# Kernel optimization log

Hardware: AMD Instinct MI355X
Metric: run time of the kernel (lower is better)

The kernel has to match this reference:

```python
import jax, jax.numpy as jnp
import numpy as np

E = 8
HID = 2048
INTER = 1408
TOT = 8192


def setup_inputs() -> dict:
    key = jax.random.key(0)
    k1, k2, k3, k4, k5 = jax.random.split(key, 5)
    # uneven token counts per expert that sum exactly to TOT (grouped-GEMM ragged sizes)
    deltas = np.array([512, -256, 128, -384, 256, -512, 384, -128], dtype=np.int32)
    tokens_per_expert = jnp.asarray(TOT // E + deltas, dtype=jnp.int32)  # sums to TOT
    permuted_x = jax.random.normal(k1, (TOT, HID), dtype=jnp.float32)
    permuted_probs = jax.random.uniform(k2, (TOT,), dtype=jnp.float32)
    s_in = 1.0 / np.sqrt(HID)
    s_mid = 1.0 / np.sqrt(INTER)
    w_gate = jax.random.normal(k3, (E, HID, INTER), dtype=jnp.float32) * s_in
    w_up = jax.random.normal(k4, (E, HID, INTER), dtype=jnp.float32) * s_in
    w_down = jax.random.normal(k5, (E, INTER, HID), dtype=jnp.float32) * s_mid
    return {
        "permuted_x": permuted_x,
        "permuted_probs": permuted_probs,
        "w_gate": w_gate,
        "w_up": w_up,
        "w_down": w_down,
        "tokens_per_expert": tokens_per_expert,
    }


def reference(permuted_x, permuted_probs, w_gate, w_up, w_down, tokens_per_expert):
    # Grouped GEMM: tokens sorted by expert; lax.ragged_dot contracts each
    # contiguous group of rows against its expert's weight without padding.
    gate = jax.lax.ragged_dot(permuted_x, w_gate, tokens_per_expert)  # [T, INTER]
    up = jax.lax.ragged_dot(permuted_x, w_up, tokens_per_expert)      # [T, INTER]
    h = jax.nn.silu(gate) * up                                         # fused SiLU-mul
    values = jax.lax.ragged_dot(h, w_down, tokens_per_expert)          # [T, HID]
    return permuted_probs[:, None].astype(values.dtype) * values
```

## Files before the change

### kernel.cpp

```cpp
#include <hip/hip_runtime.h>

typedef unsigned short u16;
typedef unsigned int u32;
typedef u16 us8 __attribute__((ext_vector_type(8)));
typedef __bf16 bf16x8 __attribute__((ext_vector_type(8)));
typedef float f32x4 __attribute__((ext_vector_type(4)));

constexpr int kE = 8;
constexpr int kHID = 2048;
constexpr int kINTER = 1408;
constexpr int kTOT = 8192;

static __device__ __forceinline__ u16 f2bf(float f) {
  u32 u = __float_as_uint(f);
  u32 r = (u + 0x7fffu + ((u >> 16) & 1u)) >> 16;
  return (u16)r;
}

static __device__ __forceinline__ void gll16(const u16* g, u16* l) {
  __builtin_amdgcn_global_load_lds(
      (const __attribute__((address_space(1))) u32*)g,
      (__attribute__((address_space(3))) u32*)l, 16, 0, 0);
}

__global__ void conv_bf16(const float* __restrict__ x, u16* __restrict__ o) {
  size_t i = ((size_t)blockIdx.x * 256 + threadIdx.x) * 8;
  const float4* p = (const float4*)(x + i);
  float4 f0 = p[0], f1 = p[1];
  us8 v;
  v[0] = f2bf(f0.x); v[1] = f2bf(f0.y); v[2] = f2bf(f0.z); v[3] = f2bf(f0.w);
  v[4] = f2bf(f1.x); v[5] = f2bf(f1.y); v[6] = f2bf(f1.z); v[7] = f2bf(f1.w);
  *(us8*)(o + i) = v;
}

__global__ void transp_bf16(const float* __restrict__ w, u16* __restrict__ wt,
                            int K, int N) {
  __shared__ float tile[64][65];
  int e = blockIdx.z;
  const float* we = w + (size_t)e * K * N;
  u16* wte = wt + (size_t)e * K * N;
  int n0 = blockIdx.x * 64, k0 = blockIdx.y * 64;
  int t = threadIdx.x;
  int kl = t >> 4, n4 = (t & 15) * 4;
#pragma unroll
  for (int r = 0; r < 4; r++) {
    int k = r * 16 + kl;
    float4 v = *(const float4*)(we + (size_t)(k0 + k) * N + n0 + n4);
    tile[k][n4 + 0] = v.x; tile[k][n4 + 1] = v.y;
    tile[k][n4 + 2] = v.z; tile[k][n4 + 3] = v.w;
  }
  __syncthreads();
#pragma unroll
  for (int r = 0; r < 2; r++) {
    int c = r * 256 + t;
    int n = c >> 3, kc = (c & 7) * 8;
    us8 o;
#pragma unroll
    for (int j = 0; j < 8; j++) o[j] = f2bf(tile[kc + j][n]);
    *(us8*)(wte + (size_t)(n0 + n) * K + k0 + kc) = o;
  }
}

static __device__ __forceinline__ bool expert_of_tile(
    const int* __restrict__ tpe, int ty, int& e, int& m0, int& m_end) {
  int tile_base = 0, row_base = 0;
  e = -1;
  for (int i = 0; i < kE; i++) {
    int tc = tpe[i];
    int nt = (tc + 127) >> 7;
    if (e < 0 && ty < tile_base + nt) {
      e = i;
      m0 = row_base + (ty - tile_base) * 128;
      m_end = row_base + tc;
    }
    tile_base += nt;
    row_base += tc;
  }
  return e >= 0;
}

__launch_bounds__(256, 2)
__global__ void gemm1(const u16* __restrict__ Xb, const u16* __restrict__ Wgt,
                      const u16* __restrict__ Wut, const float* __restrict__ probs,
                      const int* __restrict__ tpe, u16* __restrict__ H) {
  __shared__ __align__(16) u16 As[128 * 32];
  __shared__ __align__(16) u16 Bgs[128 * 32];
  __shared__ __align__(16) u16 Bus[128 * 32];

  int e, m0, m_end;
  if (!expert_of_tile(tpe, blockIdx.y, e, m0, m_end)) return;
  int n0 = blockIdx.x * 128;

  int t = threadIdx.x;
  int w = t >> 6, lane = t & 63;
  int quad = lane >> 4, l15 = lane & 15;
  int wm = (w >> 1) * 64, wn = (w & 1) * 64;

  int ar0 = m0 + (t >> 2);      if (ar0 > kTOT - 1) ar0 = kTOT - 1;
  int ar1 = m0 + 64 + (t >> 2); if (ar1 > kTOT - 1) ar1 = kTOT - 1;
  const u16* gA0 = Xb + (size_t)ar0 * kHID + (t & 3) * 8;
  const u16* gA1 = Xb + (size_t)ar1 * kHID + (t & 3) * 8;
  size_t wbase = ((size_t)e * kINTER + n0 + (t >> 2)) * kHID + (t & 3) * 8;
  const u16* gBg0 = Wgt + wbase;
  const u16* gBg1 = gBg0 + (size_t)64 * kHID;
  const u16* gBu0 = Wut + wbase;
  const u16* gBu1 = gBu0 + (size_t)64 * kHID;
  u16* lA0 = As + (size_t)(w * 64) * 8;
  u16* lA1 = As + (size_t)(256 + w * 64) * 8;
  u16* lBg0 = Bgs + (size_t)(w * 64) * 8;
  u16* lBg1 = Bgs + (size_t)(256 + w * 64) * 8;
  u16* lBu0 = Bus + (size_t)(w * 64) * 8;
  u16* lBu1 = Bus + (size_t)(256 + w * 64) * 8;

  int aoff[4], boff[4];
#pragma unroll
  for (int i = 0; i < 4; i++) aoff[i] = (wm + i * 16 + l15) * 32 + quad * 8;
#pragma unroll
  for (int j = 0; j < 4; j++) boff[j] = (wn + j * 16 + l15) * 32 + quad * 8;

  f32x4 accg[4][4] = {};
  f32x4 accu[4][4] = {};

  for (int kt = 0; kt < kHID / 32; kt++) {
    gll16(gA0, lA0);  gll16(gA1, lA1);
    gll16(gBg0, lBg0); gll16(gBg1, lBg1);
    gll16(gBu0, lBu0); gll16(gBu1, lBu1);
    gA0 += 32; gA1 += 32; gBg0 += 32; gBg1 += 32; gBu0 += 32; gBu1 += 32;
    __syncthreads();

    bf16x8 a[4], bg[4], bu[4];
#pragma unroll
    for (int i = 0; i < 4; i++) a[i] = *(const bf16x8*)(As + aoff[i]);
#pragma unroll
    for (int j = 0; j < 4; j++) {
      bg[j] = *(const bf16x8*)(Bgs + boff[j]);
      bu[j] = *(const bf16x8*)(Bus + boff[j]);
    }
#pragma unroll
    for (int i = 0; i < 4; i++)
#pragma unroll
      for (int j = 0; j < 4; j++) {
        accg[i][j] = __builtin_amdgcn_mfma_f32_16x16x32_bf16(a[i], bg[j], accg[i][j], 0, 0, 0);
        accu[i][j] = __builtin_amdgcn_mfma_f32_16x16x32_bf16(a[i], bu[j], accu[i][j], 0, 0, 0);
      }
    __syncthreads();
  }

#pragma unroll
  for (int i = 0; i < 4; i++) {
#pragma unroll
    for (int r = 0; r < 4; r++) {
      int row = m0 + wm + i * 16 + quad * 4 + r;
      if (row < m_end) {
        float p = probs[row];
#pragma unroll
        for (int j = 0; j < 4; j++) {
          int col = n0 + wn + j * 16 + l15;
          float g = accg[i][j][r], u = accu[i][j][r];
          float s = g / (1.0f + __expf(-g));
          H[(size_t)row * kINTER + col] = f2bf(s * u * p);
        }
      }
    }
  }
}

__launch_bounds__(256, 2)
__global__ void gemm2(const u16* __restrict__ H, const u16* __restrict__ Wdt,
                      const int* __restrict__ tpe, float* __restrict__ out) {
  __shared__ __align__(16) u16 As[128 * 32];
  __shared__ __align__(16) u16 Bs[128 * 32];

  int e, m0, m_end;
  if (!expert_of_tile(tpe, blockIdx.y, e, m0, m_end)) return;
  int n0 = blockIdx.x * 128;

  int t = threadIdx.x;
  int w = t >> 6, lane = t & 63;
  int quad = lane >> 4, l15 = lane & 15;
  int wm = (w >> 1) * 64, wn = (w & 1) * 64;

  int ar0 = m0 + (t >> 2);      if (ar0 > kTOT - 1) ar0 = kTOT - 1;
  int ar1 = m0 + 64 + (t >> 2); if (ar1 > kTOT - 1) ar1 = kTOT - 1;
  const u16* gA0 = H + (size_t)ar0 * kINTER + (t & 3) * 8;
  const u16* gA1 = H + (size_t)ar1 * kINTER + (t & 3) * 8;
  const u16* gB0 = Wdt + ((size_t)e * kHID + n0 + (t >> 2)) * kINTER + (t & 3) * 8;
  const u16* gB1 = gB0 + (size_t)64 * kINTER;
  u16* lA0 = As + (size_t)(w * 64) * 8;
  u16* lA1 = As + (size_t)(256 + w * 64) * 8;
  u16* lB0 = Bs + (size_t)(w * 64) * 8;
  u16* lB1 = Bs + (size_t)(256 + w * 64) * 8;

  int aoff[4], boff[4];
#pragma unroll
  for (int i = 0; i < 4; i++) aoff[i] = (wm + i * 16 + l15) * 32 + quad * 8;
#pragma unroll
  for (int j = 0; j < 4; j++) boff[j] = (wn + j * 16 + l15) * 32 + quad * 8;

  f32x4 acc[4][4] = {};

  for (int kt = 0; kt < kINTER / 32; kt++) {
    gll16(gA0, lA0); gll16(gA1, lA1);
    gll16(gB0, lB0); gll16(gB1, lB1);
    gA0 += 32; gA1 += 32; gB0 += 32; gB1 += 32;
    __syncthreads();

    bf16x8 a[4], b[4];
#pragma unroll
    for (int i = 0; i < 4; i++) a[i] = *(const bf16x8*)(As + aoff[i]);
#pragma unroll
    for (int j = 0; j < 4; j++) b[j] = *(const bf16x8*)(Bs + boff[j]);
#pragma unroll
    for (int i = 0; i < 4; i++)
#pragma unroll
      for (int j = 0; j < 4; j++)
        acc[i][j] = __builtin_amdgcn_mfma_f32_16x16x32_bf16(a[i], b[j], acc[i][j], 0, 0, 0);
    __syncthreads();
  }

#pragma unroll
  for (int i = 0; i < 4; i++) {
#pragma unroll
    for (int r = 0; r < 4; r++) {
      int row = m0 + wm + i * 16 + quad * 4 + r;
      if (row < m_end) {
#pragma unroll
        for (int j = 0; j < 4; j++) {
          int col = n0 + wn + j * 16 + l15;
          out[(size_t)row * kHID + col] = acc[i][j][r];
        }
      }
    }
  }
}

extern "C" void kernel_launch(void* const* d_in, const int* in_sizes, int n_in,
                              void* d_out, int out_size, void* d_ws, size_t ws_size,
                              hipStream_t stream) {
  const float* x = (const float*)d_in[0];
  const float* probs = (const float*)d_in[1];
  const float* wg = (const float*)d_in[2];
  const float* wu = (const float*)d_in[3];
  const float* wd = (const float*)d_in[4];
  const int* tpe = (const int*)d_in[5];
  float* out = (float*)d_out;

  u16* ws = (u16*)d_ws;
  u16* Xb = ws;
  u16* Wgt = Xb + (size_t)kTOT * kHID;
  u16* Wut = Wgt + (size_t)kE * kINTER * kHID;
  u16* Wdt = Wut + (size_t)kE * kINTER * kHID;
  u16* H = Wdt + (size_t)kE * kHID * kINTER;

  conv_bf16<<<(kTOT * kHID) / (256 * 8), 256, 0, stream>>>(x, Xb);
  transp_bf16<<<dim3(kINTER / 64, kHID / 64, kE), 256, 0, stream>>>(wg, Wgt, kHID, kINTER);
  transp_bf16<<<dim3(kINTER / 64, kHID / 64, kE), 256, 0, stream>>>(wu, Wut, kHID, kINTER);
  transp_bf16<<<dim3(kHID / 64, kINTER / 64, kE), 256, 0, stream>>>(wd, Wdt, kINTER, kHID);

  gemm1<<<dim3(kINTER / 128, 72), 256, 0, stream>>>(Xb, Wgt, Wut, probs, tpe, H);
  gemm2<<<dim3(kHID / 128, 72), 256, 0, stream>>>(H, Wdt, tpe, out);
}
```

Baseline: 571.0 us.

## Enlarge grouped GEMM tiles with 512-thread blocks for better operand reuse

Both grouped GEMMs now run eight waves per block. gemm1 uses a 256-row M tile against 128 gate/up columns, and gemm2 uses a 128x256 output tile. The global-to-LDS load mapping is rewritten so each wave fills 16 contiguous rows, and the tile-to-expert mapping takes a configurable tile height. The goal is to cut redundant weight and activation reloads per FLOP. The trade-offs are fewer blocks, which can hurt occupancy and load balance across CUs, and more ragged padding waste per expert with the 256-row tiles.

```diff
diff --git a/kernel.cpp b/kernel.cpp
--- a/kernel.cpp
+++ b/kernel.cpp
@@ -62,15 +62,16 @@
 }
 
 static __device__ __forceinline__ bool expert_of_tile(
-    const int* __restrict__ tpe, int ty, int& e, int& m0, int& m_end) {
+    const int* __restrict__ tpe, int ty, int tile_rows,
+    int& e, int& m0, int& m_end) {
   int tile_base = 0, row_base = 0;
   e = -1;
   for (int i = 0; i < kE; i++) {
     int tc = tpe[i];
-    int nt = (tc + 127) >> 7;
+    int nt = (tc + tile_rows - 1) / tile_rows;
     if (e < 0 && ty < tile_base + nt) {
       e = i;
-      m0 = row_base + (ty - tile_base) * 128;
+      m0 = row_base + (ty - tile_base) * tile_rows;
       m_end = row_base + tc;
     }
     tile_base += nt;
@@ -79,16 +80,16 @@
   return e >= 0;
 }
 
-__launch_bounds__(256, 2)
+__launch_bounds__(512, 2)
 __global__ void gemm1(const u16* __restrict__ Xb, const u16* __restrict__ Wgt,
                       const u16* __restrict__ Wut, const float* __restrict__ probs,
                       const int* __restrict__ tpe, u16* __restrict__ H) {
-  __shared__ __align__(16) u16 As[128 * 32];
+  __shared__ __align__(16) u16 As[256 * 32];
   __shared__ __align__(16) u16 Bgs[128 * 32];
   __shared__ __align__(16) u16 Bus[128 * 32];
 
   int e, m0, m_end;
-  if (!expert_of_tile(tpe, blockIdx.y, e, m0, m_end)) return;
+  if (!expert_of_tile(tpe, blockIdx.y, 256, e, m0, m_end)) return;
   int n0 = blockIdx.x * 128;
 
   int t = threadIdx.x;
@@ -96,21 +97,20 @@
   int quad = lane >> 4, l15 = lane & 15;
   int wm = (w >> 1) * 64, wn = (w & 1) * 64;
 
-  int ar0 = m0 + (t >> 2);      if (ar0 > kTOT - 1) ar0 = kTOT - 1;
-  int ar1 = m0 + 64 + (t >> 2); if (ar1 > kTOT - 1) ar1 = kTOT - 1;
-  const u16* gA0 = Xb + (size_t)ar0 * kHID + (t & 3) * 8;
-  const u16* gA1 = Xb + (size_t)ar1 * kHID + (t & 3) * 8;
-  size_t wbase = ((size_t)e * kINTER + n0 + (t >> 2)) * kHID + (t & 3) * 8;
-  const u16* gBg0 = Wgt + wbase;
-  const u16* gBg1 = gBg0 + (size_t)64 * kHID;
-  const u16* gBu0 = Wut + wbase;
-  const u16* gBu1 = gBu0 + (size_t)64 * kHID;
-  u16* lA0 = As + (size_t)(w * 64) * 8;
-  u16* lA1 = As + (size_t)(256 + w * 64) * 8;
-  u16* lBg0 = Bgs + (size_t)(w * 64) * 8;
-  u16* lBg1 = Bgs + (size_t)(256 + w * 64) * 8;
-  u16* lBu0 = Bus + (size_t)(w * 64) * 8;
-  u16* lBu1 = Bus + (size_t)(256 + w * 64) * 8;
+  int rl = w * 16 + (lane >> 2);
+  int kc8 = (lane & 3) * 8;
+
+  int ar0 = m0 + rl;        if (ar0 > kTOT - 1) ar0 = kTOT - 1;
+  int ar1 = m0 + 128 + rl;  if (ar1 > kTOT - 1) ar1 = kTOT - 1;
+  const u16* gA0 = Xb + (size_t)ar0 * kHID + kc8;
+  const u16* gA1 = Xb + (size_t)ar1 * kHID + kc8;
+  size_t wbase = ((size_t)e * kINTER + n0 + rl) * kHID + kc8;
+  const u16* gBg = Wgt + wbase;
+  const u16* gBu = Wut + wbase;
+  u16* lA0 = As + (size_t)(w * 16) * 32;
+  u16* lA1 = As + (size_t)(128 + w * 16) * 32;
+  u16* lBg = Bgs + (size_t)(w * 16) * 32;
+  u16* lBu = Bus + (size_t)(w * 16) * 32;
 
   int aoff[4], boff[4];
 #pragma unroll
@@ -122,10 +122,9 @@
   f32x4 accu[4][4] = {};
 
   for (int kt = 0; kt < kHID / 32; kt++) {
-    gll16(gA0, lA0);  gll16(gA1, lA1);
-    gll16(gBg0, lBg0); gll16(gBg1, lBg1);
-    gll16(gBu0, lBu0); gll16(gBu1, lBu1);
-    gA0 += 32; gA1 += 32; gBg0 += 32; gBg1 += 32; gBu0 += 32; gBu1 += 32;
+    gll16(gA0, lA0); gll16(gA1, lA1);
+    gll16(gBg, lBg); gll16(gBu, lBu);
+    gA0 += 32; gA1 += 32; gBg += 32; gBu += 32;
     __syncthreads();
 
     bf16x8 a[4], bg[4], bu[4];
@@ -165,31 +164,31 @@
   }
 }
 
-__launch_bounds__(256, 2)
+__launch_bounds__(512, 2)
 __global__ void gemm2(const u16* __restrict__ H, const u16* __restrict__ Wdt,
                       const int* __restrict__ tpe, float* __restrict__ out) {
   __shared__ __align__(16) u16 As[128 * 32];
-  __shared__ __align__(16) u16 Bs[128 * 32];
+  __shared__ __align__(16) u16 Bs[256 * 32];
 
   int e, m0, m_end;
-  if (!expert_of_tile(tpe, blockIdx.y, e, m0, m_end)) return;
-  int n0 = blockIdx.x * 128;
+  if (!expert_of_tile(tpe, blockIdx.y, 128, e, m0, m_end)) return;
+  int n0 = blockIdx.x * 256;
 
   int t = threadIdx.x;
   int w = t >> 6, lane = t & 63;
   int quad = lane >> 4, l15 = lane & 15;
-  int wm = (w >> 1) * 64, wn = (w & 1) * 64;
-
-  int ar0 = m0 + (t >> 2);      if (ar0 > kTOT - 1) ar0 = kTOT - 1;
-  int ar1 = m0 + 64 + (t >> 2); if (ar1 > kTOT - 1) ar1 = kTOT - 1;
-  const u16* gA0 = H + (size_t)ar0 * kINTER + (t & 3) * 8;
-  const u16* gA1 = H + (size_t)ar1 * kINTER + (t & 3) * 8;
-  const u16* gB0 = Wdt + ((size_t)e * kHID + n0 + (t >> 2)) * kINTER + (t & 3) * 8;
-  const u16* gB1 = gB0 + (size_t)64 * kINTER;
-  u16* lA0 = As + (size_t)(w * 64) * 8;
-  u16* lA1 = As + (size_t)(256 + w * 64) * 8;
-  u16* lB0 = Bs + (size_t)(w * 64) * 8;
-  u16* lB1 = Bs + (size_t)(256 + w * 64) * 8;
+  int wm = (w >> 2) * 64, wn = (w & 3) * 64;
+
+  int rl = w * 16 + (lane >> 2);
+  int kc8 = (lane & 3) * 8;
+
+  int ar = m0 + rl; if (ar > kTOT - 1) ar = kTOT - 1;
+  const u16* gA = H + (size_t)ar * kINTER + kc8;
+  const u16* gB0 = Wdt + ((size_t)e * kHID + n0 + rl) * kINTER + kc8;
+  const u16* gB1 = gB0 + (size_t)128 * kINTER;
+  u16* lA = As + (size_t)(w * 16) * 32;
+  u16* lB0 = Bs + (size_t)(w * 16) * 32;
+  u16* lB1 = Bs + (size_t)(128 + w * 16) * 32;
 
   int aoff[4], boff[4];
 #pragma unroll
@@ -200,9 +199,9 @@
   f32x4 acc[4][4] = {};
 
   for (int kt = 0; kt < kINTER / 32; kt++) {
-    gll16(gA0, lA0); gll16(gA1, lA1);
+    gll16(gA, lA);
     gll16(gB0, lB0); gll16(gB1, lB1);
-    gA0 += 32; gA1 += 32; gB0 += 32; gB1 += 32;
+    gA += 32; gB0 += 32; gB1 += 32;
     __syncthreads();
 
     bf16x8 a[4], b[4];
@@ -257,6 +256,6 @@
   transp_bf16<<<dim3(kINTER / 64, kHID / 64, kE), 256, 0, stream>>>(wu, Wut, kHID, kINTER);
   transp_bf16<<<dim3(kHID / 64, kINTER / 64, kE), 256, 0, stream>>>(wd, Wdt, kINTER, kHID);
 
-  gemm1<<<dim3(kINTER / 128, 72), 256, 0, stream>>>(Xb, Wgt, Wut, probs, tpe, H);
-  gemm2<<<dim3(kHID / 128, 72), 256, 0, stream>>>(H, Wdt, tpe, out);
-}
+  gemm1<<<dim3(kINTER / 128, 40), 512, 0, stream>>>(Xb, Wgt, Wut, probs, tpe, H);
+  gemm2<<<dim3(kHID / 256, 72), 512, 0, stream>>>(H, Wdt, tpe, out);
+}
```

After: 575.5 us. Within noise of the previous version (+0.8%).

## Double-buffer LDS tiles in both grouped GEMMs and raise occupancy hints

Applied to the files above, without the earlier changes.

Both GEMM kernels now keep two LDS buffers per operand. The next K-slice's global-to-LDS loads are issued right after the barrier, so they overlap the MFMA work on the current slice, and the trailing barrier is removed, leaving one sync per iteration. Launch bounds are raised to 3 blocks/CU for gemm1 and 4 for gemm2 to encourage more resident waves. The cost is double the LDS footprint and a tighter register budget, which may cause spills in gemm1 with its two accumulator sets.

```diff
diff --git a/kernel.cpp b/kernel.cpp
--- a/kernel.cpp
+++ b/kernel.cpp
@@ -79,13 +79,14 @@
   return e >= 0;
 }
 
-__launch_bounds__(256, 2)
+__launch_bounds__(256, 3)
 __global__ void gemm1(const u16* __restrict__ Xb, const u16* __restrict__ Wgt,
                       const u16* __restrict__ Wut, const float* __restrict__ probs,
                       const int* __restrict__ tpe, u16* __restrict__ H) {
-  __shared__ __align__(16) u16 As[128 * 32];
-  __shared__ __align__(16) u16 Bgs[128 * 32];
-  __shared__ __align__(16) u16 Bus[128 * 32];
+  constexpr int TE = 128 * 32;
+  __shared__ __align__(16) u16 As[2 * TE];
+  __shared__ __align__(16) u16 Bgs[2 * TE];
+  __shared__ __align__(16) u16 Bus[2 * TE];
 
   int e, m0, m_end;
   if (!expert_of_tile(tpe, blockIdx.y, e, m0, m_end)) return;
@@ -105,12 +106,12 @@
   const u16* gBg1 = gBg0 + (size_t)64 * kHID;
   const u16* gBu0 = Wut + wbase;
   const u16* gBu1 = gBu0 + (size_t)64 * kHID;
-  u16* lA0 = As + (size_t)(w * 64) * 8;
-  u16* lA1 = As + (size_t)(256 + w * 64) * 8;
-  u16* lBg0 = Bgs + (size_t)(w * 64) * 8;
-  u16* lBg1 = Bgs + (size_t)(256 + w * 64) * 8;
-  u16* lBu0 = Bus + (size_t)(w * 64) * 8;
-  u16* lBu1 = Bus + (size_t)(256 + w * 64) * 8;
+  u16* lA0 = As + w * 512;
+  u16* lA1 = As + 2048 + w * 512;
+  u16* lBg0 = Bgs + w * 512;
+  u16* lBg1 = Bgs + 2048 + w * 512;
+  u16* lBu0 = Bus + w * 512;
+  u16* lBu1 = Bus + 2048 + w * 512;
 
   int aoff[4], boff[4];
 #pragma unroll
@@ -121,20 +122,29 @@
   f32x4 accg[4][4] = {};
   f32x4 accu[4][4] = {};
 
-  for (int kt = 0; kt < kHID / 32; kt++) {
-    gll16(gA0, lA0);  gll16(gA1, lA1);
-    gll16(gBg0, lBg0); gll16(gBg1, lBg1);
-    gll16(gBu0, lBu0); gll16(gBu1, lBu1);
-    gA0 += 32; gA1 += 32; gBg0 += 32; gBg1 += 32; gBu0 += 32; gBu1 += 32;
+  gll16(gA0, lA0); gll16(gA1, lA1);
+  gll16(gBg0, lBg0); gll16(gBg1, lBg1);
+  gll16(gBu0, lBu0); gll16(gBu1, lBu1);
+  gA0 += 32; gA1 += 32; gBg0 += 32; gBg1 += 32; gBu0 += 32; gBu1 += 32;
+
+  constexpr int KT = kHID / 32;
+  for (int kt = 0; kt < KT; kt++) {
+    int cur = (kt & 1) ? TE : 0;
+    int nxt = TE - cur;
     __syncthreads();
-
+    if (kt + 1 < KT) {
+      gll16(gA0, lA0 + nxt); gll16(gA1, lA1 + nxt);
+      gll16(gBg0, lBg0 + nxt); gll16(gBg1, lBg1 + nxt);
+      gll16(gBu0, lBu0 + nxt); gll16(gBu1, lBu1 + nxt);
+      gA0 += 32; gA1 += 32; gBg0 += 32; gBg1 += 32; gBu0 += 32; gBu1 += 32;
+    }
     bf16x8 a[4], bg[4], bu[4];
 #pragma unroll
-    for (int i = 0; i < 4; i++) a[i] = *(const bf16x8*)(As + aoff[i]);
+    for (int i = 0; i < 4; i++) a[i] = *(const bf16x8*)(As + cur + aoff[i]);
 #pragma unroll
     for (int j = 0; j < 4; j++) {
-      bg[j] = *(const bf16x8*)(Bgs + boff[j]);
-      bu[j] = *(const bf16x8*)(Bus + boff[j]);
+      bg[j] = *(const bf16x8*)(Bgs + cur + boff[j]);
+      bu[j] = *(const bf16x8*)(Bus + cur + boff[j]);
     }
 #pragma unroll
     for (int i = 0; i < 4; i++)
@@ -143,7 +153,6 @@
         accg[i][j] = __builtin_amdgcn_mfma_f32_16x16x32_bf16(a[i], bg[j], accg[i][j], 0, 0, 0);
         accu[i][j] = __builtin_amdgcn_mfma_f32_16x16x32_bf16(a[i], bu[j], accu[i][j], 0, 0, 0);
       }
-    __syncthreads();
   }
 
 #pragma unroll
@@ -165,11 +174,12 @@
   }
 }
 
-__launch_bounds__(256, 2)
+__launch_bounds__(256, 4)
 __global__ void gemm2(const u16* __restrict__ H, const u16* __restrict__ Wdt,
                       const int* __restrict__ tpe, float* __restrict__ out) {
-  __shared__ __align__(16) u16 As[128 * 32];
-  __shared__ __align__(16) u16 Bs[128 * 32];
+  constexpr int TE = 128 * 32;
+  __shared__ __align__(16) u16 As[2 * TE];
+  __shared__ __align__(16) u16 Bs[2 * TE];
 
   int e, m0, m_end;
   if (!expert_of_tile(tpe, blockIdx.y, e, m0, m_end)) return;
@@ -186,10 +196,10 @@
   const u16* gA1 = H + (size_t)ar1 * kINTER + (t & 3) * 8;
   const u16* gB0 = Wdt + ((size_t)e * kHID + n0 + (t >> 2)) * kINTER + (t & 3) * 8;
   const u16* gB1 = gB0 + (size_t)64 * kINTER;
-  u16* lA0 = As + (size_t)(w * 64) * 8;
-  u16* lA1 = As + (size_t)(256 + w * 64) * 8;
-  u16* lB0 = Bs + (size_t)(w * 64) * 8;
-  u16* lB1 = Bs + (size_t)(256 + w * 64) * 8;
+  u16* lA0 = As + w * 512;
+  u16* lA1 = As + 2048 + w * 512;
+  u16* lB0 = Bs + w * 512;
+  u16* lB1 = Bs + 2048 + w * 512;
 
   int aoff[4], boff[4];
 #pragma unroll
@@ -199,23 +209,30 @@
 
   f32x4 acc[4][4] = {};
 
-  for (int kt = 0; kt < kINTER / 32; kt++) {
-    gll16(gA0, lA0); gll16(gA1, lA1);
-    gll16(gB0, lB0); gll16(gB1, lB1);
-    gA0 += 32; gA1 += 32; gB0 += 32; gB1 += 32;
+  gll16(gA0, lA0); gll16(gA1, lA1);
+  gll16(gB0, lB0); gll16(gB1, lB1);
+  gA0 += 32; gA1 += 32; gB0 += 32; gB1 += 32;
+
+  constexpr int KT = kINTER / 32;
+  for (int kt = 0; kt < KT; kt++) {
+    int cur = (kt & 1) ? TE : 0;
+    int nxt = TE - cur;
     __syncthreads();
-
+    if (kt + 1 < KT) {
+      gll16(gA0, lA0 + nxt); gll16(gA1, lA1 + nxt);
+      gll16(gB0, lB0 + nxt); gll16(gB1, lB1 + nxt);
+      gA0 += 32; gA1 += 32; gB0 += 32; gB1 += 32;
+    }
     bf16x8 a[4], b[4];
 #pragma unroll
-    for (int i = 0; i < 4; i++) a[i] = *(const bf16x8*)(As + aoff[i]);
-#pragma unroll
-    for (int j = 0; j < 4; j++) b[j] = *(const bf16x8*)(Bs + boff[j]);
+    for (int i = 0; i < 4; i++) a[i] = *(const bf16x8*)(As + cur + aoff[i]);
+#pragma unroll
+    for (int j = 0; j < 4; j++) b[j] = *(const bf16x8*)(Bs + cur + boff[j]);
 #pragma unroll
     for (int i = 0; i < 4; i++)
 #pragma unroll
       for (int j = 0; j < 4; j++)
         acc[i][j] = __builtin_amdgcn_mfma_f32_16x16x32_bf16(a[i], b[j], acc[i][j], 0, 0, 0);
-    __syncthreads();
   }
 
 #pragma unroll
```

Measured after the change: 677.7 us. 18.7% more time.
